# Kernel optimization log

Hardware: AMD Instinct MI355X
Metric: run time of the kernel (lower is better)

## Reference

```python
import jax, jax.numpy as jnp
import numpy as np

N_GRIDS, N_FEATS = 64, 2
GD = GH = GW = 64
PE_TERMS, N_DIMS = 6, 3
NODES, N_OUT = 64, 1
N_PTS = 524288


def setup_inputs() -> dict:
    key = jax.random.key(0)
    ks = jax.random.split(key, 8)
    x = jax.random.uniform(ks[0], (N_PTS, N_DIMS), jnp.float32, -1.0, 1.0)
    grid_scales = jax.random.uniform(ks[1], (N_GRIDS, 3), jnp.float32, 1.0, 4.0)
    grid_translations = jax.random.uniform(ks[2], (N_GRIDS, 3), jnp.float32, -1.0, 1.0) * (grid_scales - 1.0)
    feature_grids = jax.random.normal(ks[3], (N_GRIDS, N_FEATS, GD, GH, GW), jnp.float32)
    d_in = PE_TERMS * N_DIMS * 2 + N_FEATS * N_GRIDS  # 36 + 128 = 164
    W0 = jax.random.normal(ks[4], (d_in, NODES), jnp.float32) * np.sqrt(2.0 / (d_in + NODES))
    b0 = jnp.zeros((NODES,), jnp.float32)
    W1 = jax.random.normal(ks[5], (NODES, NODES), jnp.float32) * np.sqrt(2.0 / (2 * NODES))
    b1 = jnp.zeros((NODES,), jnp.float32)
    W2 = jax.random.normal(ks[6], (NODES, N_OUT), jnp.float32) * np.sqrt(2.0 / (NODES + N_OUT))
    b2 = jnp.zeros((N_OUT,), jnp.float32)
    return dict(x=x, grid_scales=grid_scales, grid_translations=grid_translations,
                feature_grids=feature_grids, W0=W0, b0=b0, W1=W1, b1=b1, W2=W2, b2=b2)


def grid_sample_3d(vol, coords):
    """Trilinear grid_sample, align_corners=True, padding_mode='zeros'.
    vol: [C,D,H,W]; coords: [N,3] in (x,y,z) order (x -> W axis), range [-1,1].
    Returns [C,N]."""
    C, D, H, W = vol.shape
    flat = vol.reshape(C, D * H * W)
    ix = (coords[:, 0] + 1.0) * 0.5 * (W - 1)
    iy = (coords[:, 1] + 1.0) * 0.5 * (H - 1)
    iz = (coords[:, 2] + 1.0) * 0.5 * (D - 1)
    x0 = jnp.floor(ix); y0 = jnp.floor(iy); z0 = jnp.floor(iz)
    wx = ix - x0; wy = iy - y0; wz = iz - z0
    x0i = x0.astype(jnp.int32); y0i = y0.astype(jnp.int32); z0i = z0.astype(jnp.int32)
    out = jnp.zeros((C, coords.shape[0]), vol.dtype)
    for dz, wz_ in ((0, 1.0 - wz), (1, wz)):
        for dy, wy_ in ((0, 1.0 - wy), (1, wy)):
            for dx, wx_ in ((0, 1.0 - wx), (1, wx)):
                xi = x0i + dx; yi = y0i + dy; zi = z0i + dz
                valid = (xi >= 0) & (xi < W) & (yi >= 0) & (yi < H) & (zi >= 0) & (zi < D)
                idx = (jnp.clip(zi, 0, D - 1) * H + jnp.clip(yi, 0, H - 1)) * W + jnp.clip(xi, 0, W - 1)
                v = jnp.take(flat, idx, axis=1) * valid.astype(vol.dtype)[None, :]
                out = out + v * (wz_ * wy_ * wx_)[None, :]
    return out


def positional_encoding(x):
    # NeRF-style PE: sin/cos of pi*2^i * x, i in [0, PE_TERMS), out dim = 2*L*3
    freqs = jnp.pi * (2.0 ** jnp.arange(PE_TERMS, dtype=jnp.float32))  # [L]
    ang = x[:, None, :] * freqs[None, :, None]                          # [N,L,3]
    n = x.shape[0]
    return jnp.concatenate([jnp.sin(ang).reshape(n, -1), jnp.cos(ang).reshape(n, -1)], axis=1)


def snake_alt(x):
    return 0.5 * x + jnp.sin(x) ** 2


def reference(x, grid_scales, grid_translations, feature_grids, W0, b0, W1, b1, W2, b2):
    # per-grid affine transform (equivalent to bmm with the scale+translation 4x4)
    tp = x[None, :, :] * grid_scales[:, None, :] + grid_translations[:, None, :]  # [G,N,3]
    feats = jax.vmap(grid_sample_3d)(feature_grids, tp)  # [G,C,N]
    G, C, N = feats.shape
    feats = feats.reshape(G * C, N).T                    # [N, G*C]
    pe = positional_encoding(x)                          # [N, 2*L*3]
    y = jnp.concatenate([pe, feats], axis=1)
    y = snake_alt(y @ W0 + b0)
    y = snake_alt(y @ W1 + b1)
    y = y @ W2 + b2
    return y
```

## Files before the change

### kernel.cpp

```cpp
#include <hip/hip_runtime.h>
#include <hip/hip_bf16.h>

#define NPTS    524288
#define NG      64
#define GSZ     64
#define VOX     (GSZ*GSZ*GSZ)
#define NODES   64
#define TILE    64
#define NBLK    (NPTS / TILE)
#define K0      192
#define SF      200
#define WLCAP   2048
#define NCELL   4096

typedef __attribute__((ext_vector_type(8))) short bf16x8;
typedef __attribute__((ext_vector_type(4))) float f32x4;

__device__ inline unsigned short f2bf(float f) {
    __hip_bfloat16 b = __float2bfloat16(f);
    union { __hip_bfloat16 h; unsigned short u; } cv; cv.h = b;
    return cv.u;
}
__device__ inline unsigned int pk2(float c0, float c1) {
    return (unsigned int)f2bf(c0) | ((unsigned int)f2bf(c1) << 16);
}
__device__ inline float bflo(unsigned int v) { return __uint_as_float(v << 16); }
__device__ inline float bfhi(unsigned int v) { return __uint_as_float(v & 0xffff0000u); }

__device__ inline int spread4(int v) {
    return (v & 1) | ((v & 2) << 2) | ((v & 4) << 4) | ((v & 8) << 6);
}
__device__ inline int cell_of(float px, float py, float pz) {
    int cx = min(max((int)((px + 1.0f) * 8.0f), 0), 15);
    int cy = min(max((int)((py + 1.0f) * 8.0f), 0), 15);
    int cz = min(max((int)((pz + 1.0f) * 8.0f), 0), 15);
    return spread4(cx) | (spread4(cy) << 1) | (spread4(cz) << 2);
}

__global__ void vox_prep(const float* __restrict__ fg, uint4* __restrict__ vox4) {
    int idx = blockIdx.x * blockDim.x + threadIdx.x;
    int g = idx >> 16;
    int v = (idx & 65535) * 4;
    const float* base = fg + (size_t)g * (2 * VOX) + v;
    float4 a = *(const float4*)base;
    float4 b = *(const float4*)(base + VOX);
    vox4[idx] = make_uint4(pk2(a.x, b.x), pk2(a.y, b.y), pk2(a.z, b.z), pk2(a.w, b.w));
}

__global__ void w_prep(const float* __restrict__ W0, const float* __restrict__ W1,
                       unsigned short* __restrict__ w0t, unsigned short* __restrict__ w1t,
                       int* __restrict__ hist) {
    int t = blockIdx.x * blockDim.x + threadIdx.x;
    hist[t] = 0;
    for (int i = t; i < NODES * K0; i += 4096) {
        int n = i / K0, k = i - n * K0;
        w0t[i] = (k < 164) ? f2bf(W0[k * NODES + n]) : (unsigned short)0;
    }
    for (int i = t; i < NODES * NODES; i += 4096) {
        int n = i >> 6, k = i & 63;
        w1t[i] = f2bf(W1[k * NODES + n]);
    }
}

__global__ void sort_count(const float* __restrict__ x, unsigned short* __restrict__ cell_id,
                           int* __restrict__ hist) {
    int p = blockIdx.x * blockDim.x + threadIdx.x;
    int c = cell_of(x[p * 3 + 0], x[p * 3 + 1], x[p * 3 + 2]);
    cell_id[p] = (unsigned short)c;
    atomicAdd(&hist[c], 1);
}

__global__ void sort_scan(const int* __restrict__ hist, int* __restrict__ offs) {
    __shared__ int partial[256];
    int t = threadIdx.x;
    int loc[16];
    int s = 0;
    #pragma unroll
    for (int i = 0; i < 16; ++i) { loc[i] = s; s += hist[t * 16 + i]; }
    partial[t] = s;
    __syncthreads();
    for (int d = 1; d < 256; d <<= 1) {
        int v = (t >= d) ? partial[t - d] : 0;
        __syncthreads();
        partial[t] += v;
        __syncthreads();
    }
    int base = partial[t] - s;
    #pragma unroll
    for (int i = 0; i < 16; ++i) offs[t * 16 + i] = base + loc[i];
}

__global__ void sort_scatter(const float* __restrict__ x, const unsigned short* __restrict__ cell_id,
                             int* __restrict__ offs, float4* __restrict__ spts) {
    int p = blockIdx.x * blockDim.x + threadIdx.x;
    int c = cell_id[p];
    int pos = atomicAdd(&offs[c], 1);
    spts[pos] = make_float4(x[p * 3 + 0], x[p * 3 + 1], x[p * 3 + 2], __int_as_float(p));
}

__device__ inline void gather_pair(int pt, int g,
                                   const unsigned int* __restrict__ vox,
                                   const float* xs, const float* gss, const float* gts,
                                   unsigned short* Fsh) {
    float px = xs[pt * 3 + 0], py = xs[pt * 3 + 1], pz = xs[pt * 3 + 2];
    float ix = (px * gss[g * 3 + 0] + gts[g * 3 + 0] + 1.0f) * 31.5f;
    float iy = (py * gss[g * 3 + 1] + gts[g * 3 + 1] + 1.0f) * 31.5f;
    float iz = (pz * gss[g * 3 + 2] + gts[g * 3 + 2] + 1.0f) * 31.5f;
    float fx = floorf(ix), fy = floorf(iy), fz = floorf(iz);
    int x0 = (int)fx, y0 = (int)fy, z0 = (int)fz;
    float wx = ix - fx, wy = iy - fy, wz = iz - fz;
    float wxa0 = (x0 >= 0) ? (1.0f - wx) : 0.0f;
    float wxa1 = (x0 < 63) ? wx : 0.0f;
    float wya0 = (y0 >= 0) ? (1.0f - wy) : 0.0f;
    float wya1 = (y0 < 63) ? wy : 0.0f;
    float wza0 = (z0 >= 0) ? (1.0f - wz) : 0.0f;
    float wza1 = (z0 < 63) ? wz : 0.0f;
    int xc0 = max(x0, 0), xc1 = min(x0 + 1, 63);
    int yc0 = max(y0, 0), yc1 = min(y0 + 1, 63);
    int zc0 = max(z0, 0), zc1 = min(z0 + 1, 63);
    const unsigned int* vg = vox + ((size_t)g << 18);
    float f0 = 0.f, f1 = 0.f;
    #pragma unroll
    for (int dz = 0; dz < 2; ++dz) {
        int zc = dz ? zc1 : zc0; float wzv = dz ? wza1 : wza0;
        #pragma unroll
        for (int dy = 0; dy < 2; ++dy) {
            int yc = dy ? yc1 : yc0; float wyv = dy ? wya1 : wya0;
            int rowb = ((zc << 6) + yc) << 6;
            float wzy = wzv * wyv;
            unsigned int v0 = vg[rowb + xc0], v1 = vg[rowb + xc1];
            f0 += wzy * (wxa0 * bflo(v0) + wxa1 * bflo(v1));
            f1 += wzy * (wxa0 * bfhi(v0) + wxa1 * bfhi(v1));
        }
    }
    *(unsigned int*)&Fsh[pt * SF + 36 + 2 * g] = pk2(f0, f1);
}

__global__ void __launch_bounds__(256, 5)
amrsrn_main(const float4* __restrict__ spts,
            const float* __restrict__ gscale,
            const float* __restrict__ gtrans,
            const unsigned int* __restrict__ vox,
            const unsigned short* __restrict__ w0t,
            const unsigned short* __restrict__ w1t,
            const float* __restrict__ b0,
            const float* __restrict__ b1,
            const float* __restrict__ W2,
            const float* __restrict__ b2,
            float* __restrict__ out) {
    __shared__ unsigned short Fsh[TILE * SF];
    __shared__ unsigned short wl[WLCAP];
    __shared__ float xs[TILE * 3];
    __shared__ int   sidx[TILE];
    __shared__ float gss[NG * 3];
    __shared__ float gts[NG * 3];
    __shared__ int wl_cnt;

    const int tid = threadIdx.x;
    const int lane = tid & 63;
    const int cb = ((blockIdx.x & 7) << 10) | (blockIdx.x >> 3);
    const int base = cb * TILE;

    for (int i = tid; i < TILE * SF / 8; i += 256) ((uint4*)Fsh)[i] = make_uint4(0,0,0,0);
    if (tid < TILE) {
        float4 sp = spts[base + tid];
        xs[tid * 3 + 0] = sp.x; xs[tid * 3 + 1] = sp.y; xs[tid * 3 + 2] = sp.z;
        sidx[tid] = __float_as_int(sp.w);
    }
    if (tid < NG * 3) { gss[tid] = gscale[tid]; gts[tid] = gtrans[tid]; }
    if (tid == 0) wl_cnt = 0;
    __syncthreads();

    {
        int pt = tid & 63;
        int grp = tid >> 6;
        #pragma unroll
        for (int t = 0; t < 9; ++t) {
            int tau = grp * 9 + t;
            int tt = (tau < 18) ? tau : tau - 18;
            int l = tt / 3, d = tt - l * 3;
            float ang = xs[pt * 3 + d] * (3.14159265358979323846f * (float)(1 << l));
            float val = (tau < 18) ? __sinf(ang) : __cosf(ang);
            Fsh[pt * SF + tau] = f2bf(val);
        }
    }

    {
        int pt = tid & 63;
        int gbase = (tid >> 6) * 16;
        float px = xs[pt * 3 + 0], py = xs[pt * 3 + 1], pz = xs[pt * 3 + 2];
        for (int gi = 0; gi < 16; ++gi) {
            int g = gbase + gi;
            float ix = (px * gss[g * 3 + 0] + gts[g * 3 + 0] + 1.0f) * 31.5f;
            float iy = (py * gss[g * 3 + 1] + gts[g * 3 + 1] + 1.0f) * 31.5f;
            float iz = (pz * gss[g * 3 + 2] + gts[g * 3 + 2] + 1.0f) * 31.5f;
            bool valid = (ix >= -1.0f) & (ix < 64.0f)
                       & (iy >= -1.0f) & (iy < 64.0f)
                       & (iz >= -1.0f) & (iz < 64.0f);
            unsigned long long m = __ballot(valid);
            if (m) {
                int b = 0;
                if (lane == 0) b = atomicAdd(&wl_cnt, __popcll(m));
                b = __shfl(b, 0);
                if (valid) {
                    int slot = b + __popcll(m & ((1ull << lane) - 1ull));
                    if (slot < WLCAP) wl[slot] = (unsigned short)((pt << 6) | g);
                    else gather_pair(pt, g, vox, xs, gss, gts, Fsh);
                }
            }
        }
    }
    __syncthreads();

    {
        int n = min(wl_cnt, WLCAP);
        for (int i = tid; i < n; i += 256) {
            int e = wl[i];
            gather_pair(e >> 6, e & 63, vox, xs, gss, gts, Fsh);
        }
    }
    __syncthreads();

    const int wv = tid >> 6;
    const int ptb = wv * 16;
    const int row = lane & 15;
    const int quad = lane >> 4;
    const int koff = quad * 8;

    f32x4 acc0[4] = {{0,0,0,0},{0,0,0,0},{0,0,0,0},{0,0,0,0}};
    #pragma unroll
    for (int ks = 0; ks < 6; ++ks) {
        bf16x8 a = *(const bf16x8*)&Fsh[(ptb + row) * SF + ks * 32 + koff];
        #pragma unroll
        for (int nt = 0; nt < 4; ++nt) {
            bf16x8 b = *(const bf16x8*)&w0t[(nt * 16 + row) * K0 + ks * 32 + koff];
            acc0[nt] = __builtin_amdgcn_mfma_f32_16x16x32_bf16(a, b, acc0[nt], 0, 0, 0);
        }
    }
    #pragma unroll
    for (int nt = 0; nt < 4; ++nt) {
        int node = nt * 16 + row;
        float bb = b0[node];
        #pragma unroll
        for (int r = 0; r < 4; ++r) {
            float h = acc0[nt][r] + bb;
            float s = __sinf(h);
            h = 0.5f * h + s * s;
            Fsh[(ptb + quad * 4 + r) * SF + node] = f2bf(h);
        }
    }

    f32x4 acc1[4] = {{0,0,0,0},{0,0,0,0},{0,0,0,0},{0,0,0,0}};
    #pragma unroll
    for (int ks = 0; ks < 2; ++ks) {
        bf16x8 a = *(const bf16x8*)&Fsh[(ptb + row) * SF + ks * 32 + koff];
        #pragma unroll
        for (int nt = 0; nt < 4; ++nt) {
            bf16x8 b = *(const bf16x8*)&w1t[(nt * 16 + row) * NODES + ks * 32 + koff];
            acc1[nt] = __builtin_amdgcn_mfma_f32_16x16x32_bf16(a, b, acc1[nt], 0, 0, 0);
        }
    }
    float part[4] = {0.f, 0.f, 0.f, 0.f};
    #pragma unroll
    for (int nt = 0; nt < 4; ++nt) {
        int node = nt * 16 + row;
        float b1v = b1[node];
        float w2v = W2[node];
        #pragma unroll
        for (int r = 0; r < 4; ++r) {
            float h = acc1[nt][r] + b1v;
            float s = __sinf(h);
            h = 0.5f * h + s * s;
            part[r] += h * w2v;
        }
    }
    #pragma unroll
    for (int m = 1; m < 16; m <<= 1) {
        #pragma unroll
        for (int r = 0; r < 4; ++r) part[r] += __shfl_xor(part[r], m);
    }
    if (row == 0) {
        float b2v = b2[0];
        #pragma unroll
        for (int r = 0; r < 4; ++r) {
            int pt = ptb + quad * 4 + r;
            out[sidx[pt]] = part[r] + b2v;
        }
    }
}

__global__ void amrsrn_fallback(const float* __restrict__ x,
                                const float* __restrict__ gscale,
                                const float* __restrict__ gtrans,
                                const float* __restrict__ fg,
                                const float* __restrict__ W0,
                                const float* __restrict__ b0,
                                const float* __restrict__ W1,
                                const float* __restrict__ b1,
                                const float* __restrict__ W2,
                                const float* __restrict__ b2,
                                float* __restrict__ out) {
    int p = blockIdx.x * blockDim.x + threadIdx.x;
    float px = x[p*3+0], py = x[p*3+1], pz = x[p*3+2];
    float h0[NODES];
    #pragma unroll
    for (int j = 0; j < NODES; ++j) h0[j] = b0[j];
    #pragma unroll
    for (int l = 0; l < 6; ++l) {
        float freq = 3.14159265358979323846f * (float)(1 << l);
        #pragma unroll
        for (int d = 0; d < 3; ++d) {
            float v = (d == 0 ? px : (d == 1 ? py : pz)) * freq;
            float s = __sinf(v), c = __cosf(v);
            const float* wrs = W0 + (l*3 + d) * NODES;
            const float* wrc = W0 + (18 + l*3 + d) * NODES;
            #pragma unroll
            for (int j = 0; j < NODES; ++j) h0[j] += s * wrs[j] + c * wrc[j];
        }
    }
    for (int g = 0; g < NG; ++g) {
        float ix = (px * gscale[g*3+0] + gtrans[g*3+0] + 1.0f) * 31.5f;
        float iy = (py * gscale[g*3+1] + gtrans[g*3+1] + 1.0f) * 31.5f;
        float iz = (pz * gscale[g*3+2] + gtrans[g*3+2] + 1.0f) * 31.5f;
        float fxf = floorf(ix), fyf = floorf(iy), fzf = floorf(iz);
        int x0 = (int)fxf, y0 = (int)fyf, z0 = (int)fzf;
        float wx = ix - fxf, wy = iy - fyf, wz = iz - fzf;
        bool any = (x0 >= -1 && x0 < GSZ) && (y0 >= -1 && y0 < GSZ) && (z0 >= -1 && z0 < GSZ);
        if (any) {
            float f0 = 0.f, f1 = 0.f;
            #pragma unroll
            for (int dz = 0; dz < 2; ++dz) {
                int zi = z0 + dz; bool vz = ((unsigned)zi < (unsigned)GSZ);
                int zc = min(max(zi, 0), GSZ - 1);
                float wzf = dz ? wz : 1.f - wz;
                #pragma unroll
                for (int dy = 0; dy < 2; ++dy) {
                    int yi = y0 + dy; bool vy = ((unsigned)yi < (unsigned)GSZ);
                    int yc = min(max(yi, 0), GSZ - 1);
                    float wyf = dy ? wy : 1.f - wy;
                    int rowoff = (zc * GSZ + yc) * GSZ;
                    #pragma unroll
                    for (int dx = 0; dx < 2; ++dx) {
                        int xi = x0 + dx; bool vx = ((unsigned)xi < (unsigned)GSZ);
                        int xc = min(max(xi, 0), GSZ - 1);
                        float w = wzf * wyf * (dx ? wx : 1.f - wx);
                        w = (vz && vy && vx) ? w : 0.f;
                        const float* gp = fg + ((size_t)g << 19);
                        f0 += w * gp[rowoff + xc];
                        f1 += w * gp[VOX + rowoff + xc];
                    }
                }
            }
            const float* wr = W0 + (36 + 2*g) * NODES;
            #pragma unroll
            for (int j = 0; j < NODES; ++j) h0[j] += f0 * wr[j] + f1 * wr[NODES + j];
        }
    }
    #pragma unroll
    for (int j = 0; j < NODES; ++j) { float s = __sinf(h0[j]); h0[j] = 0.5f * h0[j] + s * s; }
    float out_acc = b2[0];
    #pragma unroll
    for (int half = 0; half < 2; ++half) {
        float h1[32];
        #pragma unroll
        for (int j = 0; j < 32; ++j) h1[j] = b1[half*32 + j];
        #pragma unroll
        for (int i = 0; i < NODES; ++i) {
            float a = h0[i];
            const float* w1r = W1 + i * NODES + half*32;
            #pragma unroll
            for (int j = 0; j < 32; ++j) h1[j] += a * w1r[j];
        }
        #pragma unroll
        for (int j = 0; j < 32; ++j) { float s = __sinf(h1[j]); out_acc += (0.5f * h1[j] + s * s) * W2[half*32 + j]; }
    }
    out[p] = out_acc;
}

extern "C" void kernel_launch(void* const* d_in, const int* in_sizes, int n_in,
                              void* d_out, int out_size, void* d_ws, size_t ws_size,
                              hipStream_t stream) {
    const float* x      = (const float*)d_in[0];
    const float* gscale = (const float*)d_in[1];
    const float* gtrans = (const float*)d_in[2];
    const float* fg     = (const float*)d_in[3];
    const float* W0     = (const float*)d_in[4];
    const float* b0     = (const float*)d_in[5];
    const float* W1     = (const float*)d_in[6];
    const float* b1     = (const float*)d_in[7];
    const float* W2     = (const float*)d_in[8];
    const float* b2     = (const float*)d_in[9];
    float* out = (float*)d_out;

    char* wsp = (char*)d_ws;
    unsigned short* w0t = (unsigned short*)wsp;
    unsigned short* w1t = w0t + NODES * K0;
    int* hist           = (int*)(wsp + (64 << 10));
    int* offs           = (int*)(wsp + (80 << 10));
    unsigned short* cid = (unsigned short*)(wsp + (96 << 10));
    float4* spts        = (float4*)(wsp + (96 << 10) + (1 << 20));
    unsigned int* vox   = (unsigned int*)(wsp + (96 << 10) + (1 << 20) + (8 << 20));
    const size_t ws_needed = (96 << 10) + (1 << 20) + (8 << 20) + (size_t)NG * VOX * 4;

    if (ws_size >= ws_needed) {
        vox_prep<<<(NG * VOX / 4) / 256, 256, 0, stream>>>(fg, (uint4*)vox);
        w_prep<<<16, 256, 0, stream>>>(W0, W1, w0t, w1t, hist);
        sort_count<<<NPTS / 256, 256, 0, stream>>>(x, cid, hist);
        sort_scan<<<1, 256, 0, stream>>>(hist, offs);
        sort_scatter<<<NPTS / 256, 256, 0, stream>>>(x, cid, offs, spts);
        amrsrn_main<<<NBLK, 256, 0, stream>>>(spts, gscale, gtrans, vox,
                                              w0t, w1t, b0, b1, W2, b2, out);
    } else {
        amrsrn_fallback<<<NPTS / 256, 256, 0, stream>>>(
            x, gscale, gtrans, fg, W0, b0, W1, b1, W2, b2, out);
    }
}
```

Before: 471.7 us.

## Fuse prep kernels, swizzle feature LDS tile, cut shared memory for occupancy

Merges the voxel repack, weight transpose and cell-count kernels into one launch, with a memset for the histogram, and precomputes a padded grid-parameter table in global memory. The main kernel drops the shared copies of points, scales and indices, reading them from global or registers instead. It halves the worklist and switches the feature tile to an XOR-swizzled 384-byte row layout to avoid LDS bank conflicts on the MFMA A-operand loads. Together these shrink LDS use, and launch bounds are raised to 6 blocks per SM. The trade-off is extra global reads of spts and ptab in the deferred gather and output paths, and more fallback direct gathers once the smaller worklist overflows.

```diff
diff --git a/kernel.cpp b/kernel.cpp
--- a/kernel.cpp
+++ b/kernel.cpp
@@ -9,9 +9,11 @@
 #define TILE    64
 #define NBLK    (NPTS / TILE)
 #define K0      192
-#define SF      200
-#define WLCAP   2048
+#define FROW    384
+#define WLCAP   1022
 #define NCELL   4096
+#define PREP_VB 16384
+#define PREP_CB 2048
 
 typedef __attribute__((ext_vector_type(8))) short bf16x8;
 typedef __attribute__((ext_vector_type(4))) float f32x4;
@@ -26,6 +28,10 @@
 }
 __device__ inline float bflo(unsigned int v) { return __uint_as_float(v << 16); }
 __device__ inline float bfhi(unsigned int v) { return __uint_as_float(v & 0xffff0000u); }
+
+__device__ inline int fsh_addr(int row, int col2) {
+    return row * FROW + (col2 ^ ((row & 7) << 4));
+}
 
 __device__ inline int spread4(int v) {
     return (v & 1) | ((v & 2) << 2) | ((v & 4) << 4) | ((v & 8) << 6);
@@ -37,37 +43,49 @@
     return spread4(cx) | (spread4(cy) << 1) | (spread4(cz) << 2);
 }
 
-__global__ void vox_prep(const float* __restrict__ fg, uint4* __restrict__ vox4) {
-    int idx = blockIdx.x * blockDim.x + threadIdx.x;
-    int g = idx >> 16;
-    int v = (idx & 65535) * 4;
-    const float* base = fg + (size_t)g * (2 * VOX) + v;
-    float4 a = *(const float4*)base;
-    float4 b = *(const float4*)(base + VOX);
-    vox4[idx] = make_uint4(pk2(a.x, b.x), pk2(a.y, b.y), pk2(a.z, b.z), pk2(a.w, b.w));
-}
-
-__global__ void w_prep(const float* __restrict__ W0, const float* __restrict__ W1,
-                       unsigned short* __restrict__ w0t, unsigned short* __restrict__ w1t,
-                       int* __restrict__ hist) {
-    int t = blockIdx.x * blockDim.x + threadIdx.x;
-    hist[t] = 0;
-    for (int i = t; i < NODES * K0; i += 4096) {
-        int n = i / K0, k = i - n * K0;
-        w0t[i] = (k < 164) ? f2bf(W0[k * NODES + n]) : (unsigned short)0;
-    }
-    for (int i = t; i < NODES * NODES; i += 4096) {
-        int n = i >> 6, k = i & 63;
-        w1t[i] = f2bf(W1[k * NODES + n]);
-    }
-}
-
-__global__ void sort_count(const float* __restrict__ x, unsigned short* __restrict__ cell_id,
-                           int* __restrict__ hist) {
-    int p = blockIdx.x * blockDim.x + threadIdx.x;
-    int c = cell_of(x[p * 3 + 0], x[p * 3 + 1], x[p * 3 + 2]);
-    cell_id[p] = (unsigned short)c;
-    atomicAdd(&hist[c], 1);
+__global__ void prep_fused(const float* __restrict__ fg, uint4* __restrict__ vox4,
+                           const float* __restrict__ x, unsigned short* __restrict__ cid,
+                           int* __restrict__ hist,
+                           const float* __restrict__ W0, const float* __restrict__ W1,
+                           const float* __restrict__ gscale, const float* __restrict__ gtrans,
+                           unsigned short* __restrict__ w0t, unsigned short* __restrict__ w1t,
+                           float* __restrict__ ptab) {
+    int b = blockIdx.x;
+    int tid = threadIdx.x;
+    if (b < PREP_VB) {
+        int idx = b * 256 + tid;
+        int g = idx >> 16;
+        int v = (idx & 65535) * 4;
+        const float* basep = fg + (size_t)g * (2 * VOX) + v;
+        float4 a = *(const float4*)basep;
+        float4 c = *(const float4*)(basep + VOX);
+        vox4[idx] = make_uint4(pk2(a.x, c.x), pk2(a.y, c.y), pk2(a.z, c.z), pk2(a.w, c.w));
+    } else if (b < PREP_VB + PREP_CB) {
+        int p = (b - PREP_VB) * 256 + tid;
+        int c = cell_of(x[p * 3 + 0], x[p * 3 + 1], x[p * 3 + 2]);
+        cid[p] = (unsigned short)c;
+        atomicAdd(&hist[c], 1);
+    } else {
+        int t = (b - PREP_VB - PREP_CB) * 256 + tid;
+        for (int i = t; i < NODES * K0; i += 4096) {
+            int n = i / K0, k = i - n * K0;
+            w0t[i] = (k < 164) ? f2bf(W0[k * NODES + n]) : (unsigned short)0;
+        }
+        for (int i = t; i < NODES * NODES; i += 4096) {
+            int n = i >> 6, k = i & 63;
+            w1t[i] = f2bf(W1[k * NODES + n]);
+        }
+        if (t < NG) {
+            ptab[t * 8 + 0] = gscale[t * 3 + 0];
+            ptab[t * 8 + 1] = gscale[t * 3 + 1];
+            ptab[t * 8 + 2] = gscale[t * 3 + 2];
+            ptab[t * 8 + 3] = 0.0f;
+            ptab[t * 8 + 4] = gtrans[t * 3 + 0] + 1.0f;
+            ptab[t * 8 + 5] = gtrans[t * 3 + 1] + 1.0f;
+            ptab[t * 8 + 6] = gtrans[t * 3 + 2] + 1.0f;
+            ptab[t * 8 + 7] = 0.0f;
+        }
+    }
 }
 
 __global__ void sort_scan(const int* __restrict__ hist, int* __restrict__ offs) {
@@ -98,14 +116,9 @@
     spts[pos] = make_float4(x[p * 3 + 0], x[p * 3 + 1], x[p * 3 + 2], __int_as_float(p));
 }
 
-__device__ inline void gather_pair(int pt, int g,
+__device__ inline void gather_pair(int pt, int g, float ix, float iy, float iz,
                                    const unsigned int* __restrict__ vox,
-                                   const float* xs, const float* gss, const float* gts,
-                                   unsigned short* Fsh) {
-    float px = xs[pt * 3 + 0], py = xs[pt * 3 + 1], pz = xs[pt * 3 + 2];
-    float ix = (px * gss[g * 3 + 0] + gts[g * 3 + 0] + 1.0f) * 31.5f;
-    float iy = (py * gss[g * 3 + 1] + gts[g * 3 + 1] + 1.0f) * 31.5f;
-    float iz = (pz * gss[g * 3 + 2] + gts[g * 3 + 2] + 1.0f) * 31.5f;
+                                   unsigned char* FshB) {
     float fx = floorf(ix), fy = floorf(iy), fz = floorf(iz);
     int x0 = (int)fx, y0 = (int)fy, z0 = (int)fz;
     float wx = ix - fx, wy = iy - fy, wz = iz - fz;
@@ -133,13 +146,12 @@
             f1 += wzy * (wxa0 * bfhi(v0) + wxa1 * bfhi(v1));
         }
     }
-    *(unsigned int*)&Fsh[pt * SF + 36 + 2 * g] = pk2(f0, f1);
-}
-
-__global__ void __launch_bounds__(256, 5)
+    *(unsigned int*)&FshB[fsh_addr(pt, 72 + 4 * g)] = pk2(f0, f1);
+}
+
+__global__ void __launch_bounds__(256, 6)
 amrsrn_main(const float4* __restrict__ spts,
-            const float* __restrict__ gscale,
-            const float* __restrict__ gtrans,
+            const float* __restrict__ ptab,
             const unsigned int* __restrict__ vox,
             const unsigned short* __restrict__ w0t,
             const unsigned short* __restrict__ w1t,
@@ -148,64 +160,58 @@
             const float* __restrict__ W2,
             const float* __restrict__ b2,
             float* __restrict__ out) {
-    __shared__ unsigned short Fsh[TILE * SF];
-    __shared__ unsigned short wl[WLCAP];
-    __shared__ float xs[TILE * 3];
-    __shared__ int   sidx[TILE];
-    __shared__ float gss[NG * 3];
-    __shared__ float gts[NG * 3];
-    __shared__ int wl_cnt;
+    __shared__ __align__(16) unsigned char FshB[TILE * FROW];
+    __shared__ __align__(8) unsigned short wlbuf[1024];
+    int* const cntp = (int*)wlbuf;
 
     const int tid = threadIdx.x;
     const int lane = tid & 63;
     const int cb = ((blockIdx.x & 7) << 10) | (blockIdx.x >> 3);
     const int base = cb * TILE;
 
-    for (int i = tid; i < TILE * SF / 8; i += 256) ((uint4*)Fsh)[i] = make_uint4(0,0,0,0);
-    if (tid < TILE) {
-        float4 sp = spts[base + tid];
-        xs[tid * 3 + 0] = sp.x; xs[tid * 3 + 1] = sp.y; xs[tid * 3 + 2] = sp.z;
-        sidx[tid] = __float_as_int(sp.w);
-    }
-    if (tid < NG * 3) { gss[tid] = gscale[tid]; gts[tid] = gtrans[tid]; }
-    if (tid == 0) wl_cnt = 0;
+    for (int i = tid; i < TILE * FROW / 16; i += 256) ((uint4*)FshB)[i] = make_uint4(0, 0, 0, 0);
+    if (tid == 0) *cntp = 0;
+
+    const int pt = tid & 63;
+    float4 sp = spts[base + pt];
+    const float px = sp.x, py = sp.y, pz = sp.z;
     __syncthreads();
 
     {
-        int pt = tid & 63;
         int grp = tid >> 6;
         #pragma unroll
         for (int t = 0; t < 9; ++t) {
             int tau = grp * 9 + t;
             int tt = (tau < 18) ? tau : tau - 18;
             int l = tt / 3, d = tt - l * 3;
-            float ang = xs[pt * 3 + d] * (3.14159265358979323846f * (float)(1 << l));
+            float c = (d == 0) ? px : ((d == 1) ? py : pz);
+            float ang = c * (3.14159265358979323846f * (float)(1 << l));
             float val = (tau < 18) ? __sinf(ang) : __cosf(ang);
-            Fsh[pt * SF + tau] = f2bf(val);
+            *(unsigned short*)&FshB[fsh_addr(pt, tau * 2)] = f2bf(val);
         }
     }
 
     {
-        int pt = tid & 63;
         int gbase = (tid >> 6) * 16;
-        float px = xs[pt * 3 + 0], py = xs[pt * 3 + 1], pz = xs[pt * 3 + 2];
         for (int gi = 0; gi < 16; ++gi) {
             int g = gbase + gi;
-            float ix = (px * gss[g * 3 + 0] + gts[g * 3 + 0] + 1.0f) * 31.5f;
-            float iy = (py * gss[g * 3 + 1] + gts[g * 3 + 1] + 1.0f) * 31.5f;
-            float iz = (pz * gss[g * 3 + 2] + gts[g * 3 + 2] + 1.0f) * 31.5f;
+            float4 pa = *(const float4*)&ptab[g * 8];
+            float4 pb = *(const float4*)&ptab[g * 8 + 4];
+            float ix = fmaf(px, pa.x, pb.x) * 31.5f;
+            float iy = fmaf(py, pa.y, pb.y) * 31.5f;
+            float iz = fmaf(pz, pa.z, pb.z) * 31.5f;
             bool valid = (ix >= -1.0f) & (ix < 64.0f)
                        & (iy >= -1.0f) & (iy < 64.0f)
                        & (iz >= -1.0f) & (iz < 64.0f);
             unsigned long long m = __ballot(valid);
             if (m) {
                 int b = 0;
-                if (lane == 0) b = atomicAdd(&wl_cnt, __popcll(m));
+                if (lane == 0) b = atomicAdd(cntp, __popcll(m));
                 b = __shfl(b, 0);
                 if (valid) {
                     int slot = b + __popcll(m & ((1ull << lane) - 1ull));
-                    if (slot < WLCAP) wl[slot] = (unsigned short)((pt << 6) | g);
-                    else gather_pair(pt, g, vox, xs, gss, gts, Fsh);
+                    if (slot < WLCAP) wlbuf[2 + slot] = (unsigned short)((pt << 6) | g);
+                    else gather_pair(pt, g, ix, iy, iz, vox, FshB);
                 }
             }
         }
@@ -213,10 +219,17 @@
     __syncthreads();
 
     {
-        int n = min(wl_cnt, WLCAP);
+        int n = min(*cntp, WLCAP);
         for (int i = tid; i < n; i += 256) {
-            int e = wl[i];
-            gather_pair(e >> 6, e & 63, vox, xs, gss, gts, Fsh);
+            int e = wlbuf[2 + i];
+            int ept = e >> 6, eg = e & 63;
+            float4 s2 = spts[base + ept];
+            float4 pa = *(const float4*)&ptab[eg * 8];
+            float4 pb = *(const float4*)&ptab[eg * 8 + 4];
+            float ix = fmaf(s2.x, pa.x, pb.x) * 31.5f;
+            float iy = fmaf(s2.y, pa.y, pb.y) * 31.5f;
+            float iz = fmaf(s2.z, pa.z, pb.z) * 31.5f;
+            gather_pair(ept, eg, ix, iy, iz, vox, FshB);
         }
     }
     __syncthreads();
@@ -225,15 +238,14 @@
     const int ptb = wv * 16;
     const int row = lane & 15;
     const int quad = lane >> 4;
-    const int koff = quad * 8;
 
     f32x4 acc0[4] = {{0,0,0,0},{0,0,0,0},{0,0,0,0},{0,0,0,0}};
     #pragma unroll
     for (int ks = 0; ks < 6; ++ks) {
-        bf16x8 a = *(const bf16x8*)&Fsh[(ptb + row) * SF + ks * 32 + koff];
+        bf16x8 a = *(const bf16x8*)&FshB[fsh_addr(ptb + row, ks * 64 + quad * 16)];
         #pragma unroll
         for (int nt = 0; nt < 4; ++nt) {
-            bf16x8 b = *(const bf16x8*)&w0t[(nt * 16 + row) * K0 + ks * 32 + koff];
+            bf16x8 b = *(const bf16x8*)&w0t[(nt * 16 + row) * K0 + ks * 32 + quad * 8];
             acc0[nt] = __builtin_amdgcn_mfma_f32_16x16x32_bf16(a, b, acc0[nt], 0, 0, 0);
         }
     }
@@ -246,17 +258,17 @@
             float h = acc0[nt][r] + bb;
             float s = __sinf(h);
             h = 0.5f * h + s * s;
-            Fsh[(ptb + quad * 4 + r) * SF + node] = f2bf(h);
+            *(unsigned short*)&FshB[fsh_addr(ptb + quad * 4 + r, 2 * node)] = f2bf(h);
         }
     }
 
     f32x4 acc1[4] = {{0,0,0,0},{0,0,0,0},{0,0,0,0},{0,0,0,0}};
     #pragma unroll
     for (int ks = 0; ks < 2; ++ks) {
-        bf16x8 a = *(const bf16x8*)&Fsh[(ptb + row) * SF + ks * 32 + koff];
+        bf16x8 a = *(const bf16x8*)&FshB[fsh_addr(ptb + row, ks * 64 + quad * 16)];
         #pragma unroll
         for (int nt = 0; nt < 4; ++nt) {
-            bf16x8 b = *(const bf16x8*)&w1t[(nt * 16 + row) * NODES + ks * 32 + koff];
+            bf16x8 b = *(const bf16x8*)&w1t[(nt * 16 + row) * NODES + ks * 32 + quad * 8];
             acc1[nt] = __builtin_amdgcn_mfma_f32_16x16x32_bf16(a, b, acc1[nt], 0, 0, 0);
         }
     }
@@ -283,8 +295,9 @@
         float b2v = b2[0];
         #pragma unroll
         for (int r = 0; r < 4; ++r) {
-            int pt = ptb + quad * 4 + r;
-            out[sidx[pt]] = part[r] + b2v;
+            int p2 = ptb + quad * 4 + r;
+            float4 so = spts[base + p2];
+            out[__float_as_int(so.w)] = part[r] + b2v;
         }
     }
 }
@@ -395,6 +408,7 @@
     char* wsp = (char*)d_ws;
     unsigned short* w0t = (unsigned short*)wsp;
     unsigned short* w1t = w0t + NODES * K0;
+    float* ptab         = (float*)(wsp + 32768);
     int* hist           = (int*)(wsp + (64 << 10));
     int* offs           = (int*)(wsp + (80 << 10));
     unsigned short* cid = (unsigned short*)(wsp + (96 << 10));
@@ -403,12 +417,12 @@
     const size_t ws_needed = (96 << 10) + (1 << 20) + (8 << 20) + (size_t)NG * VOX * 4;
 
     if (ws_size >= ws_needed) {
-        vox_prep<<<(NG * VOX / 4) / 256, 256, 0, stream>>>(fg, (uint4*)vox);
-        w_prep<<<16, 256, 0, stream>>>(W0, W1, w0t, w1t, hist);
-        sort_count<<<NPTS / 256, 256, 0, stream>>>(x, cid, hist);
+        hipMemsetAsync(hist, 0, NCELL * sizeof(int), stream);
+        prep_fused<<<PREP_VB + PREP_CB + 16, 256, 0, stream>>>(
+            fg, (uint4*)vox, x, cid, hist, W0, W1, gscale, gtrans, w0t, w1t, ptab);
         sort_scan<<<1, 256, 0, stream>>>(hist, offs);
         sort_scatter<<<NPTS / 256, 256, 0, stream>>>(x, cid, offs, spts);
-        amrsrn_main<<<NBLK, 256, 0, stream>>>(spts, gscale, gtrans, vox,
+        amrsrn_main<<<NBLK, 256, 0, stream>>>(spts, ptab, vox,
                                               w0t, w1t, b0, b1, W2, b2, out);
     } else {
         amrsrn_fallback<<<NPTS / 256, 256, 0, stream>>>(
```

Result: slower. 499.2 us (+5.8%).

## Store voxel grid in 2x2x2 bricks and fuse prep kernels into one launch

Applied to the files above, without the earlier changes.

The packed bf16 voxel grid is reordered into 2x2x2 bricks so that the eight trilinear corner reads for a sample land in a small contiguous region (32 bytes), which should improve cache-line reuse in the gather. The voxel, histogram and weight prep kernels are merged into one launch, and the histogram is now cleared with a memset, removing launch overhead. The brick index math adds a few integer ops per lookup, and the prep reads use float2 loads instead of float4.

```diff
diff --git a/kernel.cpp b/kernel.cpp
--- a/kernel.cpp
+++ b/kernel.cpp
@@ -12,6 +12,8 @@
 #define SF      200
 #define WLCAP   2048
 #define NCELL   4096
+#define PREP_VB 16384
+#define PREP_CB 2048
 
 typedef __attribute__((ext_vector_type(8))) short bf16x8;
 typedef __attribute__((ext_vector_type(4))) float f32x4;
@@ -37,37 +39,46 @@
     return spread4(cx) | (spread4(cy) << 1) | (spread4(cz) << 2);
 }
 
-__global__ void vox_prep(const float* __restrict__ fg, uint4* __restrict__ vox4) {
-    int idx = blockIdx.x * blockDim.x + threadIdx.x;
-    int g = idx >> 16;
-    int v = (idx & 65535) * 4;
-    const float* base = fg + (size_t)g * (2 * VOX) + v;
-    float4 a = *(const float4*)base;
-    float4 b = *(const float4*)(base + VOX);
-    vox4[idx] = make_uint4(pk2(a.x, b.x), pk2(a.y, b.y), pk2(a.z, b.z), pk2(a.w, b.w));
-}
-
-__global__ void w_prep(const float* __restrict__ W0, const float* __restrict__ W1,
-                       unsigned short* __restrict__ w0t, unsigned short* __restrict__ w1t,
-                       int* __restrict__ hist) {
-    int t = blockIdx.x * blockDim.x + threadIdx.x;
-    hist[t] = 0;
-    for (int i = t; i < NODES * K0; i += 4096) {
-        int n = i / K0, k = i - n * K0;
-        w0t[i] = (k < 164) ? f2bf(W0[k * NODES + n]) : (unsigned short)0;
-    }
-    for (int i = t; i < NODES * NODES; i += 4096) {
-        int n = i >> 6, k = i & 63;
-        w1t[i] = f2bf(W1[k * NODES + n]);
-    }
-}
-
-__global__ void sort_count(const float* __restrict__ x, unsigned short* __restrict__ cell_id,
-                           int* __restrict__ hist) {
-    int p = blockIdx.x * blockDim.x + threadIdx.x;
-    int c = cell_of(x[p * 3 + 0], x[p * 3 + 1], x[p * 3 + 2]);
-    cell_id[p] = (unsigned short)c;
-    atomicAdd(&hist[c], 1);
+
+__global__ void prep_fused(const float* __restrict__ fg, uint4* __restrict__ vox4,
+                           const float* __restrict__ x, unsigned short* __restrict__ cid,
+                           int* __restrict__ hist,
+                           const float* __restrict__ W0, const float* __restrict__ W1,
+                           unsigned short* __restrict__ w0t, unsigned short* __restrict__ w1t) {
+    int b = blockIdx.x;
+    int tid = threadIdx.x;
+    if (b < PREP_VB) {
+        int idx = b * 256 + tid;
+        int g = idx >> 16;
+        int hb = idx & 65535;
+        int brick = hb >> 1;
+        int h = hb & 1;
+        int bx = brick & 31, by = (brick >> 5) & 31, bz = brick >> 10;
+        int xx = bx << 1, yy = by << 1, zz = (bz << 1) + h;
+        const float* c0 = fg + (size_t)g * (2 * VOX) + ((zz << 6) + yy) * 64 + xx;
+        const float* c1 = c0 + VOX;
+        float2 a0 = *(const float2*)c0;
+        float2 a1 = *(const float2*)(c0 + 64);
+        float2 d0 = *(const float2*)c1;
+        float2 d1 = *(const float2*)(c1 + 64);
+        vox4[idx] = make_uint4(pk2(a0.x, d0.x), pk2(a0.y, d0.y),
+                               pk2(a1.x, d1.x), pk2(a1.y, d1.y));
+    } else if (b < PREP_VB + PREP_CB) {
+        int p = (b - PREP_VB) * 256 + tid;
+        int c = cell_of(x[p * 3 + 0], x[p * 3 + 1], x[p * 3 + 2]);
+        cid[p] = (unsigned short)c;
+        atomicAdd(&hist[c], 1);
+    } else {
+        int t = (b - PREP_VB - PREP_CB) * 256 + tid;
+        for (int i = t; i < NODES * K0; i += 4096) {
+            int n = i / K0, k = i - n * K0;
+            w0t[i] = (k < 164) ? f2bf(W0[k * NODES + n]) : (unsigned short)0;
+        }
+        for (int i = t; i < NODES * NODES; i += 4096) {
+            int n = i >> 6, k = i & 63;
+            w1t[i] = f2bf(W1[k * NODES + n]);
+        }
+    }
 }
 
 __global__ void sort_scan(const int* __restrict__ hist, int* __restrict__ offs) {
@@ -118,17 +129,22 @@
     int xc0 = max(x0, 0), xc1 = min(x0 + 1, 63);
     int yc0 = max(y0, 0), yc1 = min(y0 + 1, 63);
     int zc0 = max(z0, 0), zc1 = min(z0 + 1, 63);
+    int xp0 = ((xc0 >> 1) << 3) | (xc0 & 1);
+    int xp1 = ((xc1 >> 1) << 3) | (xc1 & 1);
+    int yp0 = ((yc0 >> 1) << 8) | ((yc0 & 1) << 1);
+    int yp1 = ((yc1 >> 1) << 8) | ((yc1 & 1) << 1);
+    int zp0 = ((zc0 >> 1) << 13) | ((zc0 & 1) << 2);
+    int zp1 = ((zc1 >> 1) << 13) | ((zc1 & 1) << 2);
     const unsigned int* vg = vox + ((size_t)g << 18);
     float f0 = 0.f, f1 = 0.f;
     #pragma unroll
     for (int dz = 0; dz < 2; ++dz) {
-        int zc = dz ? zc1 : zc0; float wzv = dz ? wza1 : wza0;
+        int zp = dz ? zp1 : zp0; float wzv = dz ? wza1 : wza0;
         #pragma unroll
         for (int dy = 0; dy < 2; ++dy) {
-            int yc = dy ? yc1 : yc0; float wyv = dy ? wya1 : wya0;
-            int rowb = ((zc << 6) + yc) << 6;
-            float wzy = wzv * wyv;
-            unsigned int v0 = vg[rowb + xc0], v1 = vg[rowb + xc1];
+            int rowb = zp + (dy ? yp1 : yp0);
+            float wzy = wzv * (dy ? wya1 : wya0);
+            unsigned int v0 = vg[rowb + xp0], v1 = vg[rowb + xp1];
             f0 += wzy * (wxa0 * bflo(v0) + wxa1 * bflo(v1));
             f1 += wzy * (wxa0 * bfhi(v0) + wxa1 * bfhi(v1));
         }
@@ -403,9 +419,9 @@
     const size_t ws_needed = (96 << 10) + (1 << 20) + (8 << 20) + (size_t)NG * VOX * 4;
 
     if (ws_size >= ws_needed) {
-        vox_prep<<<(NG * VOX / 4) / 256, 256, 0, stream>>>(fg, (uint4*)vox);
-        w_prep<<<16, 256, 0, stream>>>(W0, W1, w0t, w1t, hist);
-        sort_count<<<NPTS / 256, 256, 0, stream>>>(x, cid, hist);
+        hipMemsetAsync(hist, 0, NCELL * sizeof(int), stream);
+        prep_fused<<<PREP_VB + PREP_CB + 16, 256, 0, stream>>>(
+            fg, (uint4*)vox, x, cid, hist, W0, W1, w0t, w1t);
         sort_scan<<<1, 256, 0, stream>>>(hist, offs);
         sort_scatter<<<NPTS / 256, 256, 0, stream>>>(x, cid, offs, spts);
         amrsrn_main<<<NBLK, 256, 0, stream>>>(spts, gscale, gtrans, vox,
```

Result: faster. 449.4 us (-4.7%).
